# Kernel optimization log

Hardware: AMD Instinct MI355X
Metric: run time of the kernel (lower is better)

The kernel has to match this reference:

```python
import jax, jax.numpy as jnp
import numpy as np

N_NODES = 50000
IN_DIM = 128
HID = 128
N_EDGES = 600000
BN_EPS = 1e-5


def setup_inputs() -> dict:
    key = jax.random.key(0)
    ks = jax.random.split(key, 8)
    x = jax.random.normal(ks[0], (N_NODES, IN_DIM), dtype=jnp.float32)
    edge_index = jax.random.randint(ks[1], (2, N_EDGES), 0, N_NODES, dtype=jnp.int64)
    s1 = 1.0 / np.sqrt(IN_DIM)
    s2 = 1.0 / np.sqrt(HID)
    W1 = jax.random.uniform(ks[2], (HID, IN_DIM), jnp.float32, -s1, s1)
    b1 = jax.random.uniform(ks[3], (HID,), jnp.float32, -s1, s1)
    gamma = jnp.ones((HID,), jnp.float32)
    beta = jnp.zeros((HID,), jnp.float32)
    W2 = jax.random.uniform(ks[4], (HID, HID), jnp.float32, -s2, s2)
    b2 = jax.random.uniform(ks[5], (HID,), jnp.float32, -s2, s2)
    Wres = jax.random.uniform(ks[6], (HID, IN_DIM), jnp.float32, -s1, s1)
    return {"x": x, "edge_index": edge_index, "W1": W1, "b1": b1,
            "gamma": gamma, "beta": beta, "W2": W2, "b2": b2, "Wres": Wres}


def reference(x, edge_index, W1, b1, gamma, beta, W2, b2, Wres):
    # GINConv aggregation (eps=0): h_v = x_v + sum_{u in N(v)} x_u
    src, dst = edge_index[0], edge_index[1]
    agg = jax.ops.segment_sum(x[src], dst, num_segments=N_NODES)  # [N, in_dim]
    h = x + agg
    # MLP: Linear -> BatchNorm (batch stats, training mode) -> LeakyReLU(0.01) -> Linear
    h = h @ W1.T + b1  # [N, hid]
    mu = jnp.mean(h, axis=0)
    var = jnp.mean(jnp.square(h - mu), axis=0)  # biased var, as torch BN training
    h = (h - mu) * jax.lax.rsqrt(var + BN_EPS) * gamma + beta
    h = jax.nn.leaky_relu(h, negative_slope=0.01)
    h = h @ W2.T + b2
    # residual projection + final leaky relu
    x_res = x @ Wres.T
    return jax.nn.leaky_relu(h + x_res, negative_slope=0.2)
```

## Files before the change

kernel.cpp:

```cpp
#include <hip/hip_runtime.h>

#define N_NODES 50000
#define N_EDGES 600000
#define BN_EPS 1e-5f
#define NBKT 782
#define BKT_CAP 1024
#define CHUNK 4096
#define CS_BLOCKS 147
#define CVT_BLOCKS 391

typedef __bf16 bf16x8 __attribute__((ext_vector_type(8)));
typedef float f32x4 __attribute__((ext_vector_type(4)));

__device__ __forceinline__ float leaky(float v, float slope) {
    return v > 0.f ? v : v * slope;
}

__device__ __forceinline__ bf16x8 pack8(float4 v0, float4 v1) {
    bf16x8 b;
    b[0] = (__bf16)v0.x; b[1] = (__bf16)v0.y; b[2] = (__bf16)v0.z; b[3] = (__bf16)v0.w;
    b[4] = (__bf16)v1.x; b[5] = (__bf16)v1.y; b[6] = (__bf16)v1.z; b[7] = (__bf16)v1.w;
    return b;
}

__device__ __forceinline__ void acc8(float* acc, uint4 t) {
    bf16x8 u = __builtin_bit_cast(bf16x8, t);
    #pragma unroll
    for (int k = 0; k < 8; ++k) acc[k] += (float)u[k];
}

__global__ __launch_bounds__(512) void k_fused(
        const int* __restrict__ ei, int* __restrict__ cnt, unsigned* __restrict__ coarse,
        const float4* __restrict__ x4, uint4* __restrict__ xb4,
        const float* __restrict__ W1, const float* __restrict__ W2,
        const float* __restrict__ Wres, uint4* __restrict__ w1f, uint4* __restrict__ w2f) {
    int tid = threadIdx.x;
    if (blockIdx.x == CS_BLOCKS + CVT_BLOCKS) {
        #pragma unroll
        for (int i = 0; i < 4; ++i) {
            int fid = tid + i * 512;
            int lane = fid & 63, ks = (fid >> 6) & 3, jt = fid >> 8;
            const float* wp = W1 + (jt * 16 + (lane & 15)) * 128 + ks * 32 + ((lane >> 4) << 3);
            w1f[fid] = __builtin_bit_cast(uint4, pack8(*(const float4*)wp, *(const float4*)(wp + 4)));
        }
        #pragma unroll
        for (int i = 0; i < 8; ++i) {
            int fid = tid + i * 512;
            int lane = fid & 63, ks = (fid >> 6) & 7, jt = fid >> 9;
            const float* wp = (ks < 4 ? W2 : Wres) + (jt * 16 + (lane & 15)) * 128
                              + (ks & 3) * 32 + ((lane >> 4) << 3);
            w2f[fid] = __builtin_bit_cast(uint4, pack8(*(const float4*)wp, *(const float4*)(wp + 4)));
        }
        return;
    }
    if (blockIdx.x >= CS_BLOCKS) {
        int g0 = (blockIdx.x - CS_BLOCKS) * 2048 + tid;
        #pragma unroll
        for (int i = 0; i < 4; ++i) {
            int g = g0 + i * 512;
            if (g < 800000) {
                float4 v0 = x4[g * 2], v1 = x4[g * 2 + 1];
                xb4[g] = __builtin_bit_cast(uint4, pack8(v0, v1));
            }
        }
        return;
    }
    __shared__ unsigned lcnt[NBKT];
    __shared__ unsigned lbase[NBKT];
    for (int i = tid; i < NBKT; i += 512) lcnt[i] = 0;
    __syncthreads();
    int e0 = blockIdx.x * CHUNK;
    unsigned pk[8], meta[8];
    #pragma unroll
    for (int i = 0; i < 8; ++i) {
        int e = e0 + tid + i * 512;
        if (e < N_EDGES) {
            int s = ei[e];
            int d = ei[N_EDGES + e];
            int b = d >> 6;
            pk[i] = (unsigned)s | ((unsigned)(d & 63) << 16);
            unsigned r = atomicAdd(&lcnt[b], 1u);
            meta[i] = (unsigned)b | (r << 16);
        }
    }
    __syncthreads();
    for (int b = tid; b < NBKT; b += 512) {
        unsigned c = lcnt[b];
        lbase[b] = c ? (unsigned)atomicAdd(&cnt[b], (int)c) : 0u;
    }
    __syncthreads();
    #pragma unroll
    for (int i = 0; i < 8; ++i) {
        int e = e0 + tid + i * 512;
        if (e < N_EDGES) {
            unsigned b = meta[i] & 0xFFFFu;
            unsigned p = lbase[b] + (meta[i] >> 16);
            if (p < BKT_CAP) coarse[b * BKT_CAP + p] = pk[i];
        }
    }
}

__global__ void __attribute__((amdgpu_flat_work_group_size(512, 512), amdgpu_waves_per_eu(2)))
k_agg1(
        const int* __restrict__ cnt, const unsigned* __restrict__ coarse,
        const uint4* __restrict__ xb4, const uint4* __restrict__ w1f,
        const float* __restrict__ b1, __bf16* __restrict__ h1b,
        float* __restrict__ stats) {
    __shared__ unsigned hist[64];
    __shared__ unsigned offs[64];
    __shared__ unsigned short ssrc[BKT_CAP];
    __shared__ uint4 hls[1024];
    __shared__ uint4 cls[1024];
    __shared__ float sred[8][64];
    __shared__ float s2red[8][64];
    int tid = threadIdx.x;
    int b = blockIdx.x;
    int m = cnt[b];
    if (m > BKT_CAP) m = BKT_CAP;

    int li_g = tid & 15, grp_g = tid >> 4;
    uint4 self0 = {0,0,0,0}, self1 = {0,0,0,0};
    {
        int v0n = b * 64 + grp_g;
        int v1n = b * 64 + grp_g + 32;
        if (v0n < N_NODES) self0 = xb4[v0n * 16 + li_g];
        if (v1n < N_NODES) self1 = xb4[v1n * 16 + li_g];
    }

    if (tid < 64) hist[tid] = 0;
    __syncthreads();
    unsigned pk[2], rk[2];
    #pragma unroll
    for (int i = 0; i < 2; ++i) {
        int idx = tid + i * 512;
        if (idx < m) {
            pk[i] = coarse[b * BKT_CAP + idx];
            rk[i] = atomicAdd(&hist[pk[i] >> 16], 1u);
        }
    }
    __syncthreads();
    if (tid < 64) {
        unsigned v = hist[tid];
        unsigned inc = v;
        #pragma unroll
        for (int d = 1; d < 64; d <<= 1) {
            unsigned t = __shfl_up(inc, d);
            if (tid >= d) inc += t;
        }
        offs[tid] = inc - v;
    }
    __syncthreads();
    #pragma unroll
    for (int i = 0; i < 2; ++i) {
        int idx = tid + i * 512;
        if (idx < m) ssrc[offs[pk[i] >> 16] + rk[i]] = (unsigned short)(pk[i] & 0xFFFFu);
    }
    __syncthreads();

    {
        int li = li_g, grp = grp_g;
        #pragma unroll
        for (int it = 0; it < 2; ++it) {
            int dl = grp + it * 32;
            int v = b * 64 + dl;
            if (v < N_NODES) {
                bf16x8 self = __builtin_bit_cast(bf16x8, it == 0 ? self0 : self1);
                float acc[8];
                #pragma unroll
                for (int k = 0; k < 8; ++k) acc[k] = (float)self[k];
                unsigned e0 = offs[dl], e1 = e0 + hist[dl];
                unsigned e = e0;
                for (; e + 8 <= e1; e += 8) {
                    int s0 = ssrc[e],     s1 = ssrc[e + 1], s2 = ssrc[e + 2], s3 = ssrc[e + 3];
                    int s4 = ssrc[e + 4], s5 = ssrc[e + 5], s6 = ssrc[e + 6], s7 = ssrc[e + 7];
                    uint4 t0 = xb4[s0 * 16 + li], t1 = xb4[s1 * 16 + li];
                    uint4 t2 = xb4[s2 * 16 + li], t3 = xb4[s3 * 16 + li];
                    uint4 t4 = xb4[s4 * 16 + li], t5 = xb4[s5 * 16 + li];
                    uint4 t6 = xb4[s6 * 16 + li], t7 = xb4[s7 * 16 + li];
                    acc8(acc, t0); acc8(acc, t1); acc8(acc, t2); acc8(acc, t3);
                    acc8(acc, t4); acc8(acc, t5); acc8(acc, t6); acc8(acc, t7);
                }
                if (e + 4 <= e1) {
                    int s0 = ssrc[e], s1 = ssrc[e + 1], s2 = ssrc[e + 2], s3 = ssrc[e + 3];
                    uint4 t0 = xb4[s0 * 16 + li], t1 = xb4[s1 * 16 + li];
                    uint4 t2 = xb4[s2 * 16 + li], t3 = xb4[s3 * 16 + li];
                    acc8(acc, t0); acc8(acc, t1); acc8(acc, t2); acc8(acc, t3);
                    e += 4;
                }
                for (; e < e1; ++e) {
                    acc8(acc, xb4[ssrc[e] * 16 + li]);
                }
                bf16x8 o;
                #pragma unroll
                for (int k = 0; k < 8; ++k) o[k] = (__bf16)acc[k];
                hls[dl * 16 + (li ^ (dl & 7))] = __builtin_bit_cast(uint4, o);
            }
        }
    }
    __syncthreads();

    {
        int wv = tid >> 6, lane = tid & 63;
        int rgrp = wv & 3, jh = wv >> 2;
        int node0 = b * 64 + rgrp * 16;
        bool valid = node0 < N_NODES;
        int l15 = lane & 15, q = lane >> 4;
        int dl0 = rgrp * 16 + l15;

        bf16x8 a[4];
        #pragma unroll
        for (int ks = 0; ks < 4; ++ks)
            a[ks] = __builtin_bit_cast(bf16x8, hls[dl0 * 16 + ((ks * 4 + q) ^ (dl0 & 7))]);

        __bf16* clsb = (__bf16*)cls;
        #pragma unroll
        for (int jt4 = 0; jt4 < 4; ++jt4) {
            int jt = jh * 4 + jt4;
            f32x4 acc = {0.f, 0.f, 0.f, 0.f};
            #pragma unroll
            for (int ks = 0; ks < 4; ++ks) {
                bf16x8 bb = __builtin_bit_cast(bf16x8, w1f[(jt * 4 + ks) * 64 + lane]);
                acc = __builtin_amdgcn_mfma_f32_16x16x32_bf16(a[ks], bb, acc, 0, 0, 0);
            }
            int j = jt * 16 + l15;
            float bias = b1[j];
            int c = jt * 2 + (l15 >> 3);
            int e = l15 & 7;
            float s = 0.f, s2 = 0.f;
            #pragma unroll
            for (int r = 0; r < 4; ++r) {
                float v = acc[r] + bias;
                int row = rgrp * 16 + q * 4 + r;
                clsb[(row * 16 + (c ^ (row & 7))) * 8 + e] = (__bf16)v;
                s += v; s2 += v * v;
            }
            if (!valid) { s = 0.f; s2 = 0.f; }
            s  += __shfl_down(s, 32);  s  += __shfl_down(s, 16);
            s2 += __shfl_down(s2, 32); s2 += __shfl_down(s2, 16);
            if (lane < 16) {
                sred[wv][jt4 * 16 + l15] = s;
                s2red[wv][jt4 * 16 + l15] = s2;
            }
        }
    }
    __syncthreads();

    {
        int c = tid & 15, row0 = tid >> 4;
        #pragma unroll
        for (int it = 0; it < 2; ++it) {
            int row = row0 + it * 32;
            int node = b * 64 + row;
            if (node < N_NODES)
                ((uint4*)h1b)[node * 16 + c] = cls[row * 16 + (c ^ (row & 7))];
        }
    }
    if (tid < 128) {
        int half = tid >> 6, jj = tid & 63, w0 = half * 4;
        atomicAdd(&stats[tid],
                  sred[w0][jj] + sred[w0 + 1][jj] + sred[w0 + 2][jj] + sred[w0 + 3][jj]);
        atomicAdd(&stats[128 + tid],
                  s2red[w0][jj] + s2red[w0 + 1][jj] + s2red[w0 + 2][jj] + s2red[w0 + 3][jj]);
    }
}

__global__ __launch_bounds__(256) void k_gemm2(
        const uint4* __restrict__ h1b4, const uint4* __restrict__ xb4,
        const uint4* __restrict__ w2f, const float* __restrict__ b2,
        const float* __restrict__ stats, const float* __restrict__ gamma,
        const float* __restrict__ beta, float* __restrict__ out) {
    __shared__ float bl[128], scl[128], shl[128];
    int tid = threadIdx.x;
    if (tid < 128) {
        float inv = 1.f / (float)N_NODES;
        float mu = stats[tid] * inv;
        float var = stats[128 + tid] * inv - mu * mu;
        float rs = rsqrtf(var + BN_EPS);
        float sc = gamma[tid] * rs;
        bl[tid]  = b2[tid];
        scl[tid] = sc;
        shl[tid] = beta[tid] - mu * sc;
    }
    __syncthreads();

    int wv = tid >> 6, lane = tid & 63;
    int strip = blockIdx.x * 4 + wv;
    if (strip >= 3125) return;
    int node0 = strip * 16;
    int rbase = (node0 + (lane & 15)) * 16 + (lane >> 4);
    int kbase = (lane >> 4) << 3;

    bf16x8 a[8];
    #pragma unroll
    for (int ks = 0; ks < 4; ++ks) {
        bf16x8 hv = __builtin_bit_cast(bf16x8, h1b4[rbase + ks * 4]);
        #pragma unroll
        for (int e = 0; e < 8; ++e) {
            int k = kbase + ks * 32 + e;
            float t = (float)hv[e] * scl[k] + shl[k];
            a[ks][e] = (__bf16)leaky(t, 0.01f);
        }
    }
    #pragma unroll
    for (int ks = 0; ks < 4; ++ks)
        a[4 + ks] = __builtin_bit_cast(bf16x8, xb4[rbase + ks * 4]);

    #pragma unroll
    for (int jt = 0; jt < 8; ++jt) {
        f32x4 acc = {0.f, 0.f, 0.f, 0.f};
        #pragma unroll
        for (int ks = 0; ks < 8; ++ks) {
            bf16x8 b = __builtin_bit_cast(bf16x8, w2f[(jt * 8 + ks) * 64 + lane]);
            acc = __builtin_amdgcn_mfma_f32_16x16x32_bf16(a[ks], b, acc, 0, 0, 0);
        }
        int j = jt * 16 + (lane & 15);
        float bias = bl[j];
        int nb = node0 + ((lane >> 4) << 2);
        #pragma unroll
        for (int r = 0; r < 4; ++r) {
            float v = acc[r] + bias;
            out[(nb + r) * 128 + j] = leaky(v, 0.2f);
        }
    }
}

extern "C" void kernel_launch(void* const* d_in, const int* in_sizes, int n_in,
                              void* d_out, int out_size, void* d_ws, size_t ws_size,
                              hipStream_t stream) {
    const float* x     = (const float*)d_in[0];
    const int*   ei    = (const int*)d_in[1];
    const float* W1    = (const float*)d_in[2];
    const float* b1    = (const float*)d_in[3];
    const float* gamma = (const float*)d_in[4];
    const float* beta  = (const float*)d_in[5];
    const float* W2    = (const float*)d_in[6];
    const float* b2    = (const float*)d_in[7];
    const float* Wres  = (const float*)d_in[8];
    float* out = (float*)d_out;

    char* ws = (char*)d_ws;
    uint4*    xb4    = (uint4*)ws;
    __bf16*   h1b    = (__bf16*)(ws + 25600000);
    unsigned* coarse = (unsigned*)(ws + 38400000);
    int*      cnt    = (int*)(ws + 41700000);
    float*    stats  = (float*)(ws + 41700000 + NBKT * 4);
    uint4*    w1f    = (uint4*)(ws + 42000000);
    uint4*    w2f    = w1f + 2048;

    hipMemsetAsync(cnt, 0, (NBKT + 512) * 4, stream);
    k_fused<<<CS_BLOCKS + CVT_BLOCKS + 1, 512, 0, stream>>>(ei, cnt, coarse, (const float4*)x, xb4,
                                                            W1, W2, Wres, w1f, w2f);
    k_agg1<<<NBKT, 512, 0, stream>>>(cnt, coarse, xb4, w1f, b1, h1b, stats);
    k_gemm2<<<782, 256, 0, stream>>>((const uint4*)h1b, xb4, w2f, b2, stats, gamma, beta, out);
}
```

Baseline: 89.24 us.

## Split fused aggregation+GEMM1 kernel into separate aggregation and GEMM kernels

Splits the fused kernel into two launches. k_agg does the neighbour gather-sum and writes bf16 aggregated rows to a new workspace buffer. k_gemm1 reads those rows back and runs the MFMA linear layer, bias and batch-norm statistics. The aim is to shed the large shared-memory footprint and waves_per_eu limit of the fused kernel, so the latency-bound gather runs at higher occupancy. The cost is an extra launch plus a write and re-read of roughly 12.8 MB of intermediate data.

```diff
diff --git a/kernel.cpp b/kernel.cpp
--- a/kernel.cpp
+++ b/kernel.cpp
@@ -100,147 +100,138 @@
     }
 }
 
-__global__ void __attribute__((amdgpu_flat_work_group_size(512, 512), amdgpu_waves_per_eu(2)))
-k_agg1(
+__global__ __launch_bounds__(512) void k_agg(
         const int* __restrict__ cnt, const unsigned* __restrict__ coarse,
-        const uint4* __restrict__ xb4, const uint4* __restrict__ w1f,
-        const float* __restrict__ b1, __bf16* __restrict__ h1b,
-        float* __restrict__ stats) {
+        const uint4* __restrict__ xb4, uint4* __restrict__ h4) {
     __shared__ unsigned hist[64];
     __shared__ unsigned offs[64];
     __shared__ unsigned short ssrc[BKT_CAP];
-    __shared__ uint4 hls[1024];
+    int tid = threadIdx.x;
+    int b = blockIdx.x;
+    int m = cnt[b];
+    if (m > BKT_CAP) m = BKT_CAP;
+
+    if (tid < 64) hist[tid] = 0;
+    __syncthreads();
+    unsigned pk[2], rk[2];
+    #pragma unroll
+    for (int i = 0; i < 2; ++i) {
+        int idx = tid + i * 512;
+        if (idx < m) {
+            pk[i] = coarse[b * BKT_CAP + idx];
+            rk[i] = atomicAdd(&hist[pk[i] >> 16], 1u);
+        }
+    }
+    __syncthreads();
+    if (tid < 64) {
+        unsigned v = hist[tid];
+        unsigned inc = v;
+        #pragma unroll
+        for (int d = 1; d < 64; d <<= 1) {
+            unsigned t = __shfl_up(inc, d);
+            if (tid >= d) inc += t;
+        }
+        offs[tid] = inc - v;
+    }
+    __syncthreads();
+    #pragma unroll
+    for (int i = 0; i < 2; ++i) {
+        int idx = tid + i * 512;
+        if (idx < m) ssrc[offs[pk[i] >> 16] + rk[i]] = (unsigned short)(pk[i] & 0xFFFFu);
+    }
+    __syncthreads();
+
+    int li = tid & 15, grp = tid >> 4;
+    #pragma unroll
+    for (int it = 0; it < 2; ++it) {
+        int dl = grp + it * 32;
+        int v = b * 64 + dl;
+        if (v >= N_NODES) continue;
+        float acc[8];
+        {
+            bf16x8 self = __builtin_bit_cast(bf16x8, xb4[v * 16 + li]);
+            #pragma unroll
+            for (int k = 0; k < 8; ++k) acc[k] = (float)self[k];
+        }
+        unsigned e0 = offs[dl], e1 = e0 + hist[dl];
+        unsigned e = e0;
+        for (; e + 8 <= e1; e += 8) {
+            int s0 = ssrc[e],     s1 = ssrc[e + 1], s2 = ssrc[e + 2], s3 = ssrc[e + 3];
+            int s4 = ssrc[e + 4], s5 = ssrc[e + 5], s6 = ssrc[e + 6], s7 = ssrc[e + 7];
+            uint4 t0 = xb4[s0 * 16 + li], t1 = xb4[s1 * 16 + li];
+            uint4 t2 = xb4[s2 * 16 + li], t3 = xb4[s3 * 16 + li];
+            uint4 t4 = xb4[s4 * 16 + li], t5 = xb4[s5 * 16 + li];
+            uint4 t6 = xb4[s6 * 16 + li], t7 = xb4[s7 * 16 + li];
+            acc8(acc, t0); acc8(acc, t1); acc8(acc, t2); acc8(acc, t3);
+            acc8(acc, t4); acc8(acc, t5); acc8(acc, t6); acc8(acc, t7);
+        }
+        if (e + 4 <= e1) {
+            int s0 = ssrc[e], s1 = ssrc[e + 1], s2 = ssrc[e + 2], s3 = ssrc[e + 3];
+            uint4 t0 = xb4[s0 * 16 + li], t1 = xb4[s1 * 16 + li];
+            uint4 t2 = xb4[s2 * 16 + li], t3 = xb4[s3 * 16 + li];
+            acc8(acc, t0); acc8(acc, t1); acc8(acc, t2); acc8(acc, t3);
+            e += 4;
+        }
+        for (; e < e1; ++e) {
+            acc8(acc, xb4[ssrc[e] * 16 + li]);
+        }
+        bf16x8 o;
+        #pragma unroll
+        for (int k = 0; k < 8; ++k) o[k] = (__bf16)acc[k];
+        h4[v * 16 + li] = __builtin_bit_cast(uint4, o);
+    }
+}
+
+__global__ __launch_bounds__(512) void k_gemm1(
+        const uint4* __restrict__ h4, const uint4* __restrict__ w1f,
+        const float* __restrict__ b1, __bf16* __restrict__ h1b,
+        float* __restrict__ stats) {
     __shared__ uint4 cls[1024];
     __shared__ float sred[8][64];
     __shared__ float s2red[8][64];
     int tid = threadIdx.x;
     int b = blockIdx.x;
-    int m = cnt[b];
-    if (m > BKT_CAP) m = BKT_CAP;
-
-    int li_g = tid & 15, grp_g = tid >> 4;
-    uint4 self0 = {0,0,0,0}, self1 = {0,0,0,0};
-    {
-        int v0n = b * 64 + grp_g;
-        int v1n = b * 64 + grp_g + 32;
-        if (v0n < N_NODES) self0 = xb4[v0n * 16 + li_g];
-        if (v1n < N_NODES) self1 = xb4[v1n * 16 + li_g];
-    }
-
-    if (tid < 64) hist[tid] = 0;
-    __syncthreads();
-    unsigned pk[2], rk[2];
-    #pragma unroll
-    for (int i = 0; i < 2; ++i) {
-        int idx = tid + i * 512;
-        if (idx < m) {
-            pk[i] = coarse[b * BKT_CAP + idx];
-            rk[i] = atomicAdd(&hist[pk[i] >> 16], 1u);
-        }
-    }
-    __syncthreads();
-    if (tid < 64) {
-        unsigned v = hist[tid];
-        unsigned inc = v;
-        #pragma unroll
-        for (int d = 1; d < 64; d <<= 1) {
-            unsigned t = __shfl_up(inc, d);
-            if (tid >= d) inc += t;
-        }
-        offs[tid] = inc - v;
-    }
-    __syncthreads();
-    #pragma unroll
-    for (int i = 0; i < 2; ++i) {
-        int idx = tid + i * 512;
-        if (idx < m) ssrc[offs[pk[i] >> 16] + rk[i]] = (unsigned short)(pk[i] & 0xFFFFu);
-    }
-    __syncthreads();
-
-    {
-        int li = li_g, grp = grp_g;
-        #pragma unroll
-        for (int it = 0; it < 2; ++it) {
-            int dl = grp + it * 32;
-            int v = b * 64 + dl;
-            if (v < N_NODES) {
-                bf16x8 self = __builtin_bit_cast(bf16x8, it == 0 ? self0 : self1);
-                float acc[8];
-                #pragma unroll
-                for (int k = 0; k < 8; ++k) acc[k] = (float)self[k];
-                unsigned e0 = offs[dl], e1 = e0 + hist[dl];
-                unsigned e = e0;
-                for (; e + 8 <= e1; e += 8) {
-                    int s0 = ssrc[e],     s1 = ssrc[e + 1], s2 = ssrc[e + 2], s3 = ssrc[e + 3];
-                    int s4 = ssrc[e + 4], s5 = ssrc[e + 5], s6 = ssrc[e + 6], s7 = ssrc[e + 7];
-                    uint4 t0 = xb4[s0 * 16 + li], t1 = xb4[s1 * 16 + li];
-                    uint4 t2 = xb4[s2 * 16 + li], t3 = xb4[s3 * 16 + li];
-                    uint4 t4 = xb4[s4 * 16 + li], t5 = xb4[s5 * 16 + li];
-                    uint4 t6 = xb4[s6 * 16 + li], t7 = xb4[s7 * 16 + li];
-                    acc8(acc, t0); acc8(acc, t1); acc8(acc, t2); acc8(acc, t3);
-                    acc8(acc, t4); acc8(acc, t5); acc8(acc, t6); acc8(acc, t7);
-                }
-                if (e + 4 <= e1) {
-                    int s0 = ssrc[e], s1 = ssrc[e + 1], s2 = ssrc[e + 2], s3 = ssrc[e + 3];
-                    uint4 t0 = xb4[s0 * 16 + li], t1 = xb4[s1 * 16 + li];
-                    uint4 t2 = xb4[s2 * 16 + li], t3 = xb4[s3 * 16 + li];
-                    acc8(acc, t0); acc8(acc, t1); acc8(acc, t2); acc8(acc, t3);
-                    e += 4;
-                }
-                for (; e < e1; ++e) {
-                    acc8(acc, xb4[ssrc[e] * 16 + li]);
-                }
-                bf16x8 o;
-                #pragma unroll
-                for (int k = 0; k < 8; ++k) o[k] = (__bf16)acc[k];
-                hls[dl * 16 + (li ^ (dl & 7))] = __builtin_bit_cast(uint4, o);
-            }
-        }
-    }
-    __syncthreads();
-
-    {
-        int wv = tid >> 6, lane = tid & 63;
-        int rgrp = wv & 3, jh = wv >> 2;
-        int node0 = b * 64 + rgrp * 16;
-        bool valid = node0 < N_NODES;
-        int l15 = lane & 15, q = lane >> 4;
-        int dl0 = rgrp * 16 + l15;
-
-        bf16x8 a[4];
-        #pragma unroll
-        for (int ks = 0; ks < 4; ++ks)
-            a[ks] = __builtin_bit_cast(bf16x8, hls[dl0 * 16 + ((ks * 4 + q) ^ (dl0 & 7))]);
-
-        __bf16* clsb = (__bf16*)cls;
-        #pragma unroll
-        for (int jt4 = 0; jt4 < 4; ++jt4) {
-            int jt = jh * 4 + jt4;
-            f32x4 acc = {0.f, 0.f, 0.f, 0.f};
-            #pragma unroll
-            for (int ks = 0; ks < 4; ++ks) {
-                bf16x8 bb = __builtin_bit_cast(bf16x8, w1f[(jt * 4 + ks) * 64 + lane]);
-                acc = __builtin_amdgcn_mfma_f32_16x16x32_bf16(a[ks], bb, acc, 0, 0, 0);
-            }
-            int j = jt * 16 + l15;
-            float bias = b1[j];
-            int c = jt * 2 + (l15 >> 3);
-            int e = l15 & 7;
-            float s = 0.f, s2 = 0.f;
-            #pragma unroll
-            for (int r = 0; r < 4; ++r) {
-                float v = acc[r] + bias;
-                int row = rgrp * 16 + q * 4 + r;
-                clsb[(row * 16 + (c ^ (row & 7))) * 8 + e] = (__bf16)v;
-                s += v; s2 += v * v;
-            }
-            if (!valid) { s = 0.f; s2 = 0.f; }
-            s  += __shfl_down(s, 32);  s  += __shfl_down(s, 16);
-            s2 += __shfl_down(s2, 32); s2 += __shfl_down(s2, 16);
-            if (lane < 16) {
-                sred[wv][jt4 * 16 + l15] = s;
-                s2red[wv][jt4 * 16 + l15] = s2;
-            }
+
+    int wv = tid >> 6, lane = tid & 63;
+    int rgrp = wv & 3, jh = wv >> 2;
+    int node0 = b * 64 + rgrp * 16;
+    bool valid = node0 < N_NODES;
+    int l15 = lane & 15, q = lane >> 4;
+
+    bf16x8 a[4];
+    int rbase = (node0 + l15) * 16 + q;
+    #pragma unroll
+    for (int ks = 0; ks < 4; ++ks)
+        a[ks] = __builtin_bit_cast(bf16x8, h4[rbase + ks * 4]);
+
+    __bf16* clsb = (__bf16*)cls;
+    #pragma unroll
+    for (int jt4 = 0; jt4 < 4; ++jt4) {
+        int jt = jh * 4 + jt4;
+        f32x4 acc = {0.f, 0.f, 0.f, 0.f};
+        #pragma unroll
+        for (int ks = 0; ks < 4; ++ks) {
+            bf16x8 bb = __builtin_bit_cast(bf16x8, w1f[(jt * 4 + ks) * 64 + lane]);
+            acc = __builtin_amdgcn_mfma_f32_16x16x32_bf16(a[ks], bb, acc, 0, 0, 0);
+        }
+        int j = jt * 16 + l15;
+        float bias = b1[j];
+        int c = jt * 2 + (l15 >> 3);
+        int e = l15 & 7;
+        float s = 0.f, s2 = 0.f;
+        #pragma unroll
+        for (int r = 0; r < 4; ++r) {
+            float v = acc[r] + bias;
+            int row = rgrp * 16 + q * 4 + r;
+            clsb[(row * 16 + (c ^ (row & 7))) * 8 + e] = (__bf16)v;
+            s += v; s2 += v * v;
+        }
+        if (!valid) { s = 0.f; s2 = 0.f; }
+        s  += __shfl_down(s, 32);  s  += __shfl_down(s, 16);
+        s2 += __shfl_down(s2, 32); s2 += __shfl_down(s2, 16);
+        if (lane < 16) {
+            sred[wv][jt4 * 16 + l15] = s;
+            s2red[wv][jt4 * 16 + l15] = s2;
         }
     }
     __syncthreads();
@@ -340,6 +331,7 @@
 
     char* ws = (char*)d_ws;
     uint4*    xb4    = (uint4*)ws;
+    uint4*    h4     = (uint4*)(ws + 12800000);
     __bf16*   h1b    = (__bf16*)(ws + 25600000);
     unsigned* coarse = (unsigned*)(ws + 38400000);
     int*      cnt    = (int*)(ws + 41700000);
@@ -350,6 +342,7 @@
     hipMemsetAsync(cnt, 0, (NBKT + 512) * 4, stream);
     k_fused<<<CS_BLOCKS + CVT_BLOCKS + 1, 512, 0, stream>>>(ei, cnt, coarse, (const float4*)x, xb4,
                                                             W1, W2, Wres, w1f, w2f);
-    k_agg1<<<NBKT, 512, 0, stream>>>(cnt, coarse, xb4, w1f, b1, h1b, stats);
+    k_agg<<<NBKT, 512, 0, stream>>>(cnt, coarse, xb4, h4);
+    k_gemm1<<<NBKT, 512, 0, stream>>>(h4, w1f, b1, h1b, stats);
     k_gemm2<<<782, 256, 0, stream>>>((const uint4*)h1b, xb4, w2f, b2, stats, gamma, beta, out);
 }
```

After: 103.9 us. +16.5%, slower.
